# Kernel tuning notes

Hardware: AMD Instinct MI355X
Metric: run time of the kernel (lower is better)

The kernel has to match this reference:

```python
import jax, jax.numpy as jnp
import numpy as np

B, S, D = 8, 1024, 512          # batch, seq_len, d_model
H, HD = 8, 64                   # num_heads, head_dim (D = H*HD)
L = 128                         # latent_dim
LH = L // H                     # latent_head_dim = 16
M_ALPHA = -1e9                  # additive mask coefficient


def setup_inputs() -> dict:
    key = jax.random.key(0)
    ks = jax.random.split(key, 9)
    s = 0.02
    return {
        "x": jax.random.normal(ks[0], (B, S, D), jnp.float32),
        "mask": jax.random.uniform(ks[1], (B, S, 1), jnp.float32),  # (B,S,1) single-column mask
        "Wq": jax.random.normal(ks[2], (D, D), jnp.float32) * s,
        "bq": jnp.zeros((D,), jnp.float32),
        "Wckv": jax.random.normal(ks[3], (D, L), jnp.float32) * s,   # latent KV compression
        "Wuk": jax.random.normal(ks[4], (L, D), jnp.float32) * s,    # key up-proj (absorbed into q)
        "Wuv": jax.random.normal(ks[5], (L, D), jnp.float32) * s,    # value up-proj
        "Wo": jax.random.normal(ks[6], (D, D), jnp.float32) * s,
        "bo": jnp.zeros((D,), jnp.float32),
    }


def reference(x, mask, Wq, bq, Wckv, Wuk, Wuv, Wo, bo):
    b, s, d = x.shape
    # Q path: full query then project into latent space via Wuk^T (weight absorption)
    q_full = x @ Wq + bq                              # (B,S,D)
    q_lat = q_full @ Wuk.T                            # (B,S,L)
    q = q_lat.reshape(b, s, H, LH).transpose(0, 2, 1, 3)      # (B,H,S,LH)
    # K/V path: compressed latent KV
    k_lat_full = x @ Wckv                             # (B,S,L)
    k = k_lat_full.reshape(b, s, H, LH).transpose(0, 2, 1, 3)  # (B,H,S,LH)
    v_full = k_lat_full @ Wuv                         # (B,S,D)
    v = v_full.reshape(b, s, H, HD).transpose(0, 2, 1, 3)      # (B,H,S,HD)
    # scaled dot-product in latent space (dk = latent_head_dim)
    logits = jnp.einsum('bhqd,bhkd->bhqk', q, k) / jnp.sqrt(jnp.float32(LH))
    qk_values = logits
    # 'QK' mask: tile single-column (B,S,1)->(B,S,S), symmetrize, clamp at 1
    m = jnp.broadcast_to(mask, (b, s, s))             # tile along keys
    m = m + m.transpose(0, 2, 1)                      # symmetric (square case)
    m = jnp.minimum(1.0, m)
    logits = logits + m[:, None, :, :] * M_ALPHA      # (B,H,S,S)
    attn_weights = jax.nn.softmax(logits, axis=-1)
    attn = jnp.einsum('bhqk,bhkd->bhqd', attn_weights, v)      # (B,H,S,HD)
    attn = attn.transpose(0, 2, 1, 3).reshape(b, s, d)         # merge heads
    out = attn @ Wo + bo                              # (B,S,D)
    return out, attn_weights, qk_values
```

## Files before the change

### kernel.cpp

```cpp
#include <hip/hip_runtime.h>
#include <hip/hip_bf16.h>

typedef __hip_bfloat16 bf16;
typedef __attribute__((ext_vector_type(8))) short short8;
typedef __attribute__((ext_vector_type(4))) float f32x4;

#define B_ 8
#define S_ 1024
#define D_ 512
#define H_ 8
#define HD_ 64
#define L_ 128
#define LH_ 16

__device__ __forceinline__ float bfu2f(unsigned short u) {
  unsigned int x = ((unsigned int)u) << 16;
  float f;
  __builtin_memcpy(&f, &x, 4);
  return f;
}
__device__ __forceinline__ unsigned short bfbits(float f) {
  bf16 h = __float2bfloat16(f);
  unsigned short u;
  __builtin_memcpy(&u, &h, 2);
  return u;
}
__device__ __forceinline__ f32x4 mfma_bf16(short8 a, short8 b, f32x4 c) {
  return __builtin_amdgcn_mfma_f32_16x16x32_bf16(a, b, c, 0, 0, 0);
}


template<bool BT, bool BIAS, bool ABF16, bool CBF16>
__global__ __launch_bounds__(256) void gemm(const void* __restrict__ Ap, int lda,
                                            const void* __restrict__ Bp, int ldb,
                                            void* __restrict__ Cp, int ldc,
                                            const float* __restrict__ bias, int K) {
  __shared__ float As[16][65];
  __shared__ float Bs[16][65];
  const int tid = threadIdx.x;
  const int m0 = blockIdx.y * 64, n0 = blockIdx.x * 64;
  const int ty = tid >> 4, tx = tid & 15;
  float acc[4][4] = {};
  for (int kt = 0; kt < K; kt += 16) {
    {
      const int m = tid >> 2, kq = (tid & 3) * 4;
      if (ABF16) {
        const bf16* A = (const bf16*)Ap;
        ushort4 u = *reinterpret_cast<const ushort4*>(
            reinterpret_cast<const unsigned short*>(A) + (size_t)(m0 + m) * lda + kt + kq);
        As[kq + 0][m] = bfu2f(u.x);
        As[kq + 1][m] = bfu2f(u.y);
        As[kq + 2][m] = bfu2f(u.z);
        As[kq + 3][m] = bfu2f(u.w);
      } else {
        const float* A = (const float*)Ap;
        float4 v = *reinterpret_cast<const float4*>(A + (size_t)(m0 + m) * lda + kt + kq);
        As[kq + 0][m] = v.x;
        As[kq + 1][m] = v.y;
        As[kq + 2][m] = v.z;
        As[kq + 3][m] = v.w;
      }
    }
    if (BT) {
      const int n = tid >> 2, kq = (tid & 3) * 4;
      const float* Bf = (const float*)Bp;
      float4 v = *reinterpret_cast<const float4*>(Bf + (size_t)(n0 + n) * ldb + kt + kq);
      Bs[kq + 0][n] = v.x;
      Bs[kq + 1][n] = v.y;
      Bs[kq + 2][n] = v.z;
      Bs[kq + 3][n] = v.w;
    } else {
      const int k = tid >> 4, nq = (tid & 15) * 4;
      const float* Bf = (const float*)Bp;
      float4 v = *reinterpret_cast<const float4*>(Bf + (size_t)(kt + k) * ldb + n0 + nq);
      Bs[k][nq + 0] = v.x;
      Bs[k][nq + 1] = v.y;
      Bs[k][nq + 2] = v.z;
      Bs[k][nq + 3] = v.w;
    }
    __syncthreads();
#pragma unroll
    for (int k = 0; k < 16; ++k) {
      float a0 = As[k][ty * 4 + 0], a1 = As[k][ty * 4 + 1];
      float a2 = As[k][ty * 4 + 2], a3 = As[k][ty * 4 + 3];
      float b0 = Bs[k][tx * 4 + 0], b1 = Bs[k][tx * 4 + 1];
      float b2 = Bs[k][tx * 4 + 2], b3 = Bs[k][tx * 4 + 3];
      acc[0][0] += a0 * b0; acc[0][1] += a0 * b1; acc[0][2] += a0 * b2; acc[0][3] += a0 * b3;
      acc[1][0] += a1 * b0; acc[1][1] += a1 * b1; acc[1][2] += a1 * b2; acc[1][3] += a1 * b3;
      acc[2][0] += a2 * b0; acc[2][1] += a2 * b1; acc[2][2] += a2 * b2; acc[2][3] += a2 * b3;
      acc[3][0] += a3 * b0; acc[3][1] += a3 * b1; acc[3][2] += a3 * b2; acc[3][3] += a3 * b3;
    }
    __syncthreads();
  }
#pragma unroll
  for (int i = 0; i < 4; ++i)
#pragma unroll
    for (int j = 0; j < 4; ++j) {
      const size_t row = m0 + ty * 4 + i;
      const int col = n0 + tx * 4 + j;
      float v = acc[i][j];
      if (BIAS) v += bias[col];
      if (CBF16)
        reinterpret_cast<bf16*>(Cp)[row * ldc + col] = __float2bfloat16(v);
      else
        reinterpret_cast<float*>(Cp)[row * ldc + col] = v;
    }
}

__global__ __launch_bounds__(256) void k_conv(const float* __restrict__ in,
                                              bf16* __restrict__ out, int n) {
  int i = (blockIdx.x * 256 + threadIdx.x) * 4;
  if (i >= n) return;
  float4 v = *reinterpret_cast<const float4*>(in + i);
  ushort4 o = { bfbits(v.x), bfbits(v.y), bfbits(v.z), bfbits(v.w) };
  *reinterpret_cast<ushort4*>(out + i) = o;
}

__global__ __launch_bounds__(256) void k_tr_f32_bf16(const float* __restrict__ in,
                                                     bf16* __restrict__ out,
                                                     int R, int C) {
  __shared__ float t[32][33];
  int tx = threadIdx.x & 31, ty = threadIdx.x >> 5;
  int r0 = blockIdx.y * 32, c0 = blockIdx.x * 32;
#pragma unroll
  for (int i = 0; i < 32; i += 8)
    t[ty + i][tx] = in[(size_t)(r0 + ty + i) * C + c0 + tx];
  __syncthreads();
#pragma unroll
  for (int i = 0; i < 32; i += 8)
    out[(size_t)(c0 + ty + i) * R + r0 + tx] = __float2bfloat16(t[tx][ty + i]);
}

__global__ __launch_bounds__(256) void k_copy_wckv(const float* __restrict__ Wckv,
                                                   float* __restrict__ wcat) {
  int idx = blockIdx.x * 256 + threadIdx.x;
  int k = idx >> 7, n = idx & 127;
  wcat[k * 256 + 128 + n] = Wckv[k * 128 + n];
}

__global__ __launch_bounds__(64) void k_biascomb(const float* __restrict__ bq,
                                                 const float* __restrict__ Wuk,
                                                 float* __restrict__ bias_c) {
  int j = blockIdx.x, lane = threadIdx.x;
  if (j >= L_) { if (lane == 0) bias_c[j] = 0.f; return; }
  float s = 0.f;
  for (int d = lane; d < D_; d += 64) s += bq[d] * Wuk[j * D_ + d];
#pragma unroll
  for (int off = 32; off > 0; off >>= 1) s += __shfl_down(s, off);
  if (lane == 0) bias_c[j] = s;
}

template<int LDA, int LDB, int LDC, int KK, bool CBF16, bool BIAS>
__global__ __launch_bounds__(256) void gemm_mfma_t(const bf16* __restrict__ Ab,
                                                   const bf16* __restrict__ Bt,
                                                   void* __restrict__ Cp,
                                                   const float* __restrict__ bias) {
  __shared__ __align__(16) short sA[128 * 40];
  __shared__ __align__(16) short sB[128 * 40];
  const int tid = threadIdx.x, lane = tid & 63;
  const int l15 = lane & 15, l4 = lane >> 4;
  const int wm = ((tid >> 6) >> 1) * 64, wn = ((tid >> 6) & 1) * 64;
  const size_t bn0 = (size_t)blockIdx.x * 128, bm0 = (size_t)blockIdx.y * 128;
  const unsigned short* A = reinterpret_cast<const unsigned short*>(Ab);
  const unsigned short* Bu = reinterpret_cast<const unsigned short*>(Bt);
  f32x4 acc[4][4] = {};
  for (int kt = 0; kt < KK; kt += 32) {
    __syncthreads();
#pragma unroll
    for (int i = 0; i < 2; ++i) {
      const int c = tid + i * 256;
      const int row = c >> 2, k8 = (c & 3) * 8;
      *reinterpret_cast<uint4*>(&sA[row * 40 + k8]) =
          *reinterpret_cast<const uint4*>(A + (bm0 + row) * LDA + kt + k8);
      *reinterpret_cast<uint4*>(&sB[row * 40 + k8]) =
          *reinterpret_cast<const uint4*>(Bu + (bn0 + row) * LDB + kt + k8);
    }
    __syncthreads();
    short8 av[4], bv[4];
#pragma unroll
    for (int mf = 0; mf < 4; ++mf)
      av[mf] = *reinterpret_cast<const short8*>(&sA[(wm + mf * 16 + l15) * 40 + l4 * 8]);
#pragma unroll
    for (int nf = 0; nf < 4; ++nf)
      bv[nf] = *reinterpret_cast<const short8*>(&sB[(wn + nf * 16 + l15) * 40 + l4 * 8]);
#pragma unroll
    for (int mf = 0; mf < 4; ++mf)
#pragma unroll
      for (int nf = 0; nf < 4; ++nf)
        acc[mf][nf] = mfma_bf16(av[mf], bv[nf], acc[mf][nf]);
  }
#pragma unroll
  for (int mf = 0; mf < 4; ++mf)
#pragma unroll
    for (int nf = 0; nf < 4; ++nf)
#pragma unroll
      for (int j = 0; j < 4; ++j) {
        const size_t row = bm0 + wm + mf * 16 + l4 * 4 + j;
        const int col = bn0 + wn + nf * 16 + l15;
        float v = acc[mf][nf][j];
        if (BIAS) v += bias[col];
        if (CBF16)
          reinterpret_cast<bf16*>(Cp)[row * LDC + col] = __float2bfloat16(v);
        else
          reinterpret_cast<float*>(Cp)[row * LDC + col] = v;
      }
}

__global__ __launch_bounds__(512) void k_qk3w(const float* __restrict__ xw,
                                              const float* __restrict__ maskg,
                                              float* __restrict__ qk_out,
                                              float* __restrict__ aw_out) {
  __shared__ __align__(16) float Kl[512 * 20];
  __shared__ float mkl[S_];
  __shared__ float qls[16 * 16];
  const int bh = blockIdx.y, b = bh >> 3, h = bh & 7;
  const int q0 = blockIdx.x * 16;
  const int tid = threadIdx.x, w = tid >> 6, lane = tid & 63;

  for (int i = tid; i < S_; i += 512) mkl[i] = maskg[b * S_ + i];
  if (tid < 64) {
    const int row = tid >> 2, qq = (tid & 3) * 4;
    float4 v = *reinterpret_cast<const float4*>(
        xw + (size_t)(b * S_ + q0 + row) * 256 + h * LH_ + qq);
    qls[row * 16 + qq + 0] = v.x; qls[row * 16 + qq + 1] = v.y;
    qls[row * 16 + qq + 2] = v.z; qls[row * 16 + qq + 3] = v.w;
  }
  __syncthreads();

  const int r0 = w * 2;
  float qr[2][16], mq[2];
#pragma unroll
  for (int r = 0; r < 2; ++r) {
#pragma unroll
    for (int t = 0; t < 16; ++t) qr[r][t] = qls[(r0 + r) * 16 + t];
    mq[r] = mkl[q0 + r0 + r];
  }
  const size_t obase = (size_t)bh * S_ * S_;
  float l[2][16];

#pragma unroll
  for (int half = 0; half < 2; ++half) {
    if (half) __syncthreads();
#pragma unroll
    for (int i = 0; i < 4; ++i) {
      const int idx = tid + i * 512;
      const int key = idx >> 2, qq = (idx & 3) * 4;
      float4 v = *reinterpret_cast<const float4*>(
          xw + (size_t)(b * S_ + half * 512 + key) * 256 + 128 + h * LH_ + qq);
      *reinterpret_cast<float4*>(&Kl[key * 20 + qq]) = v;
    }
    __syncthreads();
#pragma unroll
    for (int c = 0; c < 8; ++c) {
      const int lkey = c * 64 + lane;
      const int key = half * 512 + lkey;
      float kv[16];
#pragma unroll
      for (int t = 0; t < 16; t += 4) {
        float4 v = *reinterpret_cast<const float4*>(&Kl[lkey * 20 + t]);
        kv[t] = v.x; kv[t + 1] = v.y; kv[t + 2] = v.z; kv[t + 3] = v.w;
      }
      const float mk = mkl[key];
#pragma unroll
      for (int r = 0; r < 2; ++r) {
        float d = 0.f;
#pragma unroll
        for (int t = 0; t < 16; ++t) d += qr[r][t] * kv[t];
        d *= 0.25f;
        qk_out[obase + (size_t)(q0 + r0 + r) * S_ + key] = d;
        const float m = fminf(1.f, __fadd_rn(mq[r], mk));
        l[r][half * 8 + c] = __fadd_rn(d, __fmul_rn(m, -1e9f));
      }
    }
  }

#pragma unroll
  for (int r = 0; r < 2; ++r) {
    float M = l[r][0];
#pragma unroll
    for (int idx = 1; idx < 16; ++idx) M = fmaxf(M, l[r][idx]);
#pragma unroll
    for (int st = 1; st < 64; st <<= 1) M = fmaxf(M, __shfl_xor(M, st));
    float s = 0.f;
#pragma unroll
    for (int idx = 0; idx < 16; ++idx) {
      const float e = __expf(l[r][idx] - M);
      l[r][idx] = e;
      s += e;
    }
#pragma unroll
    for (int st = 1; st < 64; st <<= 1) s += __shfl_xor(s, st);
    const float inv = 1.f / s;
    const size_t orow = obase + (size_t)(q0 + r0 + r) * S_;
#pragma unroll
    for (int idx = 0; idx < 16; ++idx)
      aw_out[orow + (idx >> 3) * 512 + (idx & 7) * 64 + lane] = l[r][idx] * inv;
  }
}

__global__ __launch_bounds__(256) void k_pv_mfma(const float* __restrict__ aw,
                                                 const bf16* __restrict__ vt,
                                                 bf16* __restrict__ attn) {
  __shared__ __align__(16) short Pl[128 * 40];
  __shared__ __align__(16) short Vl[64 * 40];
  const int bh = blockIdx.y, b = bh >> 3, h = bh & 7;
  const int q0 = blockIdx.x * 128;
  const int tid = threadIdx.x, w = tid >> 6, lane = tid & 63;
  const int l15 = lane & 15, l4 = lane >> 4;
  const float* A = aw + (size_t)bh * S_ * S_;
  const unsigned short* vtp =
      reinterpret_cast<const unsigned short*>(vt) + (size_t)h * 64 * 8192 + b * S_;
  f32x4 acc[2][4] = {};
  for (int kt = 0; kt < 32; ++kt) {
    __syncthreads();
    {
      const int r = tid >> 1, half = (tid & 1) * 16;
      const float* src = A + (size_t)(q0 + r) * S_ + kt * 32 + half;
      short* dst = &Pl[r * 40 + half];
#pragma unroll
      for (int i = 0; i < 4; ++i) {
        float4 v = *reinterpret_cast<const float4*>(src + i * 4);
        ushort4 o = { bfbits(v.x), bfbits(v.y), bfbits(v.z), bfbits(v.w) };
        *reinterpret_cast<ushort4*>(dst + i * 4) = o;
      }
    }
    if (tid < 64) {
      const unsigned short* src = vtp + (size_t)tid * 8192 + kt * 32;
      *reinterpret_cast<uint4*>(&Vl[tid * 40 + 0])  = *reinterpret_cast<const uint4*>(src + 0);
      *reinterpret_cast<uint4*>(&Vl[tid * 40 + 8])  = *reinterpret_cast<const uint4*>(src + 8);
      *reinterpret_cast<uint4*>(&Vl[tid * 40 + 16]) = *reinterpret_cast<const uint4*>(src + 16);
      *reinterpret_cast<uint4*>(&Vl[tid * 40 + 24]) = *reinterpret_cast<const uint4*>(src + 24);
    }
    __syncthreads();
    short8 av[2], bv[4];
#pragma unroll
    for (int mf = 0; mf < 2; ++mf)
      av[mf] = *reinterpret_cast<const short8*>(&Pl[(w * 32 + mf * 16 + l15) * 40 + l4 * 8]);
#pragma unroll
    for (int nf = 0; nf < 4; ++nf)
      bv[nf] = *reinterpret_cast<const short8*>(&Vl[(nf * 16 + l15) * 40 + l4 * 8]);
#pragma unroll
    for (int mf = 0; mf < 2; ++mf)
#pragma unroll
      for (int nf = 0; nf < 4; ++nf)
        acc[mf][nf] = mfma_bf16(av[mf], bv[nf], acc[mf][nf]);
  }
#pragma unroll
  for (int mf = 0; mf < 2; ++mf)
#pragma unroll
    for (int nf = 0; nf < 4; ++nf)
#pragma unroll
      for (int j = 0; j < 4; ++j)
        attn[(size_t)(b * S_ + q0 + w * 32 + mf * 16 + l4 * 4 + j) * 512 +
             h * 64 + nf * 16 + l15] = __float2bfloat16(acc[mf][nf][j]);
}

__global__ __launch_bounds__(256) void gemm_mfma_out(const bf16* __restrict__ Ab,
                                                     const bf16* __restrict__ Bt,
                                                     float* __restrict__ C,
                                                     const float* __restrict__ bias) {
  __shared__ __align__(16) short sA[128 * 40];
  __shared__ __align__(16) short sB[128 * 40];
  const int tid = threadIdx.x, lane = tid & 63;
  const int l15 = lane & 15, l4 = lane >> 4;
  const int wm = ((tid >> 6) >> 1) * 64, wn = ((tid >> 6) & 1) * 64;
  const size_t bn0 = (size_t)blockIdx.x * 128, bm0 = (size_t)blockIdx.y * 128;
  const unsigned short* A = reinterpret_cast<const unsigned short*>(Ab);
  const unsigned short* Bu = reinterpret_cast<const unsigned short*>(Bt);
  f32x4 acc[4][4] = {};
  for (int kt = 0; kt < 512; kt += 32) {
    __syncthreads();
#pragma unroll
    for (int i = 0; i < 2; ++i) {
      const int c = tid + i * 256;
      const int row = c >> 2, k8 = (c & 3) * 8;
      *reinterpret_cast<uint4*>(&sA[row * 40 + k8]) =
          *reinterpret_cast<const uint4*>(A + (bm0 + row) * 512 + kt + k8);
      *reinterpret_cast<uint4*>(&sB[row * 40 + k8]) =
          *reinterpret_cast<const uint4*>(Bu + (bn0 + row) * 512 + kt + k8);
    }
    __syncthreads();
    short8 av[4], bv[4];
#pragma unroll
    for (int mf = 0; mf < 4; ++mf)
      av[mf] = *reinterpret_cast<const short8*>(&sA[(wm + mf * 16 + l15) * 40 + l4 * 8]);
#pragma unroll
    for (int nf = 0; nf < 4; ++nf)
      bv[nf] = *reinterpret_cast<const short8*>(&sB[(wn + nf * 16 + l15) * 40 + l4 * 8]);
#pragma unroll
    for (int mf = 0; mf < 4; ++mf)
#pragma unroll
      for (int nf = 0; nf < 4; ++nf)
        acc[mf][nf] = mfma_bf16(av[mf], bv[nf], acc[mf][nf]);
  }
#pragma unroll
  for (int mf = 0; mf < 4; ++mf)
#pragma unroll
    for (int nf = 0; nf < 4; ++nf)
#pragma unroll
      for (int j = 0; j < 4; ++j) {
        const size_t row = bm0 + wm + mf * 16 + l4 * 4 + j;
        const int col = bn0 + wn + nf * 16 + l15;
        C[row * 512 + col] = acc[mf][nf][j] + bias[col];
      }
}

extern "C" void kernel_launch(void* const* d_in, const int* in_sizes, int n_in,
                              void* d_out, int out_size, void* d_ws, size_t ws_size,
                              hipStream_t stream) {
  const float* x    = (const float*)d_in[0];
  const float* mask = (const float*)d_in[1];
  const float* Wq   = (const float*)d_in[2];
  const float* bq   = (const float*)d_in[3];
  const float* Wckv = (const float*)d_in[4];
  const float* Wuk  = (const float*)d_in[5];
  const float* Wuv  = (const float*)d_in[6];
  const float* Wo   = (const float*)d_in[7];
  const float* bo   = (const float*)d_in[8];

  float* out    = (float*)d_out;
  float* aw_out = out + (size_t)B_ * S_ * D_;
  float* qk_out = aw_out + (size_t)B_ * H_ * S_ * S_;

  uint8_t* p = (uint8_t*)d_ws;
  auto alloc = [&](size_t bytes) {
    void* r = p;
    p += (bytes + 255) & ~(size_t)255;
    return r;
  };
  float* wcat    = (float*)alloc((size_t)512 * 256 * 4);
  float* bias_c  = (float*)alloc(256 * 4);
  bf16*  wcatT   = (bf16*)alloc((size_t)256 * 512 * 2);
  bf16*  wuvT_bf = (bf16*)alloc((size_t)512 * 128 * 2);
  bf16*  woT     = (bf16*)alloc((size_t)512 * 512 * 2);
  bf16*  x_bf    = (bf16*)alloc((size_t)8192 * 512 * 2);
  float* xw      = (float*)alloc((size_t)8192 * 256 * 4);
  bf16*  xw_bf   = (bf16*)alloc((size_t)8192 * 256 * 2);
  bf16*  vt      = (bf16*)alloc((size_t)512 * 8192 * 2);
  bf16*  attn_bf = (bf16*)xw;

  gemm<true, false, false, false><<<dim3(2, 8), 256, 0, stream>>>(
      Wq, 512, Wuk, 512, wcat, 256, nullptr, 512);
  k_copy_wckv<<<256, 256, 0, stream>>>(Wckv, wcat);
  k_biascomb<<<256, 64, 0, stream>>>(bq, Wuk, bias_c);
  k_tr_f32_bf16<<<dim3(8, 16), 256, 0, stream>>>(wcat, wcatT, 512, 256);
  k_tr_f32_bf16<<<dim3(16, 4), 256, 0, stream>>>(Wuv, wuvT_bf, 128, 512);
  k_tr_f32_bf16<<<dim3(16, 16), 256, 0, stream>>>(Wo, woT, 512, 512);
  k_conv<<<4096, 256, 0, stream>>>(x, x_bf, 8192 * 512);
  gemm_mfma_t<512, 512, 256, 512, false, true><<<dim3(2, 64), 256, 0, stream>>>(
      x_bf, wcatT, xw, bias_c);
  k_conv<<<2048, 256, 0, stream>>>(xw, xw_bf, 8192 * 256);
  gemm_mfma_t<128, 256, 8192, 128, true, false><<<dim3(64, 4), 256, 0, stream>>>(
      wuvT_bf, xw_bf + 128, vt, nullptr);
  k_qk3w<<<dim3(64, 64), 512, 0, stream>>>(xw, mask, qk_out, aw_out);
  k_pv_mfma<<<dim3(8, 64), 256, 0, stream>>>(aw_out, vt, attn_bf);
  gemm_mfma_out<<<dim3(4, 64), 256, 0, stream>>>(attn_bf, woT, out, bo);
  (void)in_sizes; (void)n_in; (void)out_size; (void)ws_size;
}
```

Baseline: 318.9 us.

## Transpose K tile in LDS and vectorize QK logits and softmax stores

The QK/softmax kernel now loads all 1024 keys for the head at once into a transposed LDS layout (dimension-major, padded rows) instead of two key-major halves. Each lane computes four consecutive keys per group, which allows float4 LDS reads, float4 mask reads and float4 global stores of both the qk logits and the attention weights. The goal is to cut store instruction count and improve coalescing on the two large S×S outputs, which dominate memory traffic. In exchange LDS use per block roughly doubles (about 64KB), which may lower occupancy, and the transposed LDS write pattern uses scalar stores that may conflict.

```diff
diff --git a/kernel.cpp b/kernel.cpp
--- a/kernel.cpp
+++ b/kernel.cpp
@@ -206,12 +206,12 @@
       }
 }
 
-__global__ __launch_bounds__(512) void k_qk3w(const float* __restrict__ xw,
-                                              const float* __restrict__ maskg,
-                                              float* __restrict__ qk_out,
-                                              float* __restrict__ aw_out) {
-  __shared__ __align__(16) float Kl[512 * 20];
-  __shared__ float mkl[S_];
+__global__ __launch_bounds__(512) void k_qk4(const float* __restrict__ xw,
+                                             const float* __restrict__ maskg,
+                                             float* __restrict__ qk_out,
+                                             float* __restrict__ aw_out) {
+  __shared__ __align__(16) float Kl[16 * 1028];
+  __shared__ __align__(16) float mkl[S_];
   __shared__ float qls[16 * 16];
   const int bh = blockIdx.y, b = bh >> 3, h = bh & 7;
   const int q0 = blockIdx.x * 16;
@@ -225,6 +225,17 @@
     qls[row * 16 + qq + 0] = v.x; qls[row * 16 + qq + 1] = v.y;
     qls[row * 16 + qq + 2] = v.z; qls[row * 16 + qq + 3] = v.w;
   }
+#pragma unroll
+  for (int i = 0; i < 8; ++i) {
+    const int idx = tid + i * 512;
+    const int key = idx >> 2, qq = (idx & 3) * 4;
+    float4 v = *reinterpret_cast<const float4*>(
+        xw + (size_t)(b * S_ + key) * 256 + 128 + h * LH_ + qq);
+    Kl[(qq + 0) * 1028 + key] = v.x;
+    Kl[(qq + 1) * 1028 + key] = v.y;
+    Kl[(qq + 2) * 1028 + key] = v.z;
+    Kl[(qq + 3) * 1028 + key] = v.w;
+  }
   __syncthreads();
 
   const int r0 = w * 2;
@@ -239,38 +250,31 @@
   float l[2][16];
 
 #pragma unroll
-  for (int half = 0; half < 2; ++half) {
-    if (half) __syncthreads();
-#pragma unroll
-    for (int i = 0; i < 4; ++i) {
-      const int idx = tid + i * 512;
-      const int key = idx >> 2, qq = (idx & 3) * 4;
-      float4 v = *reinterpret_cast<const float4*>(
-          xw + (size_t)(b * S_ + half * 512 + key) * 256 + 128 + h * LH_ + qq);
-      *reinterpret_cast<float4*>(&Kl[key * 20 + qq]) = v;
-    }
-    __syncthreads();
-#pragma unroll
-    for (int c = 0; c < 8; ++c) {
-      const int lkey = c * 64 + lane;
-      const int key = half * 512 + lkey;
-      float kv[16];
-#pragma unroll
-      for (int t = 0; t < 16; t += 4) {
-        float4 v = *reinterpret_cast<const float4*>(&Kl[lkey * 20 + t]);
-        kv[t] = v.x; kv[t + 1] = v.y; kv[t + 2] = v.z; kv[t + 3] = v.w;
+  for (int g = 0; g < 4; ++g) {
+    const int key = g * 256 + lane * 4;
+    float acc[2][4] = {};
+#pragma unroll
+    for (int t = 0; t < 16; ++t) {
+      float4 kv = *reinterpret_cast<const float4*>(&Kl[t * 1028 + key]);
+      acc[0][0] += qr[0][t] * kv.x; acc[0][1] += qr[0][t] * kv.y;
+      acc[0][2] += qr[0][t] * kv.z; acc[0][3] += qr[0][t] * kv.w;
+      acc[1][0] += qr[1][t] * kv.x; acc[1][1] += qr[1][t] * kv.y;
+      acc[1][2] += qr[1][t] * kv.z; acc[1][3] += qr[1][t] * kv.w;
+    }
+    const float4 mkv = *reinterpret_cast<const float4*>(&mkl[key]);
+    const float mk4[4] = { mkv.x, mkv.y, mkv.z, mkv.w };
+#pragma unroll
+    for (int r = 0; r < 2; ++r) {
+      float4 qv;
+      float* qvp = reinterpret_cast<float*>(&qv);
+#pragma unroll
+      for (int j = 0; j < 4; ++j) {
+        const float d = acc[r][j] * 0.25f;
+        qvp[j] = d;
+        const float m = fminf(1.f, __fadd_rn(mq[r], mk4[j]));
+        l[r][g * 4 + j] = __fadd_rn(d, __fmul_rn(m, -1e9f));
       }
-      const float mk = mkl[key];
-#pragma unroll
-      for (int r = 0; r < 2; ++r) {
-        float d = 0.f;
-#pragma unroll
-        for (int t = 0; t < 16; ++t) d += qr[r][t] * kv[t];
-        d *= 0.25f;
-        qk_out[obase + (size_t)(q0 + r0 + r) * S_ + key] = d;
-        const float m = fminf(1.f, __fadd_rn(mq[r], mk));
-        l[r][half * 8 + c] = __fadd_rn(d, __fmul_rn(m, -1e9f));
-      }
+      *reinterpret_cast<float4*>(qk_out + obase + (size_t)(q0 + r0 + r) * S_ + key) = qv;
     }
   }
 
@@ -293,8 +297,11 @@
     const float inv = 1.f / s;
     const size_t orow = obase + (size_t)(q0 + r0 + r) * S_;
 #pragma unroll
-    for (int idx = 0; idx < 16; ++idx)
-      aw_out[orow + (idx >> 3) * 512 + (idx & 7) * 64 + lane] = l[r][idx] * inv;
+    for (int g = 0; g < 4; ++g) {
+      float4 o = { l[r][g * 4 + 0] * inv, l[r][g * 4 + 1] * inv,
+                   l[r][g * 4 + 2] * inv, l[r][g * 4 + 3] * inv };
+      *reinterpret_cast<float4*>(aw_out + orow + g * 256 + lane * 4) = o;
+    }
   }
 }
 
@@ -452,7 +459,7 @@
   k_conv<<<2048, 256, 0, stream>>>(xw, xw_bf, 8192 * 256);
   gemm_mfma_t<128, 256, 8192, 128, true, false><<<dim3(64, 4), 256, 0, stream>>>(
       wuvT_bf, xw_bf + 128, vt, nullptr);
-  k_qk3w<<<dim3(64, 64), 512, 0, stream>>>(xw, mask, qk_out, aw_out);
+  k_qk4<<<dim3(64, 64), 512, 0, stream>>>(xw, mask, qk_out, aw_out);
   k_pv_mfma<<<dim3(8, 64), 256, 0, stream>>>(aw_out, vt, attn_bf);
   gemm_mfma_out<<<dim3(4, 64), 256, 0, stream>>>(attn_bf, woT, out, bo);
   (void)in_sizes; (void)n_in; (void)out_size; (void)ws_size;
```

New measurement: 324.7 us. No clear change (+1.8%).
